# Kernel optimization log

Hardware: AMD Instinct MI355X
Metric: run time of the kernel (lower is better)

Reference implementation:

```python
import jax, jax.numpy as jnp
import numpy as np

B, S, IN, N, OUT = 4, 4096, 1024, 1024, 1024  # state_size == num_heads, head_dim = 1, hippo D = 1


def setup_inputs() -> dict:
    key = jax.random.key(0)
    ks = jax.random.split(key, 6)
    x = jax.random.normal(ks[0], (B, S, IN), dtype=jnp.float32)
    # input_projection: Linear(input_size, state_size, bias=True)
    Wi = jax.random.normal(ks[1], (IN, N), dtype=jnp.float32) / np.sqrt(IN)
    bi = jax.random.normal(ks[2], (N,), dtype=jnp.float32) * 0.01
    # state_weight (N,1,1) -> per-head scalar recurrence weight; hippo_weight (N,1) -> per-head scalar
    w = jax.random.normal(ks[3], (N,), dtype=jnp.float32)
    u = jax.random.normal(ks[4], (N,), dtype=jnp.float32)
    # output_projection: Linear(state_size, output_size, bias=False)
    Wo = jax.random.normal(ks[5], (N, OUT), dtype=jnp.float32) / np.sqrt(N)
    input_state = jnp.zeros((B, N), dtype=jnp.float32)         # (B, N, H=1) squeezed
    hippo_state = jnp.zeros((B, N, 1, 1), dtype=jnp.float32)   # (B, N, H=1, D=1)
    return {"x": x, "Wi": Wi, "bi": bi, "w": w, "u": u, "Wo": Wo,
            "input_state": input_state, "hippo_state": hippo_state}


def reference(x, Wi, bi, w, u, Wo, input_state, hippo_state):
    # input projection then split into N heads of dim 1 -> [B, S, N]
    xp = jnp.einsum("bsi,in->bsn", x, Wi) + bi
    # hippo cross-term: (hippo_state @ hippo_weight) with H=D=1 -> scalar per (b, n).
    # hippo_state is never updated inside the recurrence (torch path), so this is constant over time.
    hippo_term = hippo_state[..., 0, 0] * u  # [B, N]

    def step(h, xt):
        # h_t = tanh(h_{t-1} * w + x_t + hippo_term)   (per-head scalar recurrence, H=1)
        h = jnp.tanh(h * w + xt + hippo_term)
        return h, h

    xs = jnp.swapaxes(xp, 0, 1)  # [S, B, N]
    last_state, ys = jax.lax.scan(step, input_state, xs)
    states = jnp.swapaxes(ys, 0, 1)  # [B, S, N]
    out = jnp.einsum("bsn,no->bso", states, Wo)  # output_projection (no bias)
    output_state = last_state.reshape(B, -1)     # input[:, -1] flattened over (N, H)
    return out, output_state
```

## Files before the change

### kernel.cpp

```cpp
#include <hip/hip_runtime.h>
#include <hip/hip_bf16.h>

using f16x8 = __attribute__((ext_vector_type(8))) _Float16;
using f32x4 = __attribute__((ext_vector_type(4))) float;

extern "C" __device__ float __ocml_native_exp2_f32(float);

static constexpr int Bc = 4, Sc = 4096, INc = 1024, Nc = 1024, OUTc = 1024;
static constexpr int Mc = Bc * Sc;
#define K2LE 2.8853900817779268f

__device__ __forceinline__ unsigned short f2h(float f) {
    return __builtin_bit_cast(unsigned short, (_Float16)f);
}
__device__ __forceinline__ float h2f(unsigned short s) {
    return (float)__builtin_bit_cast(_Float16, s);
}

__global__ __launch_bounds__(256) void split2h(const float* __restrict__ in,
                                               unsigned short* __restrict__ hi,
                                               unsigned short* __restrict__ lo, int n4) {
    int i = blockIdx.x * blockDim.x + threadIdx.x;
    if (i >= n4) return;
    float4 v = reinterpret_cast<const float4*>(in)[i];
    ushort4 h, l;
    h.x = f2h(v.x); l.x = f2h(v.x - h2f(h.x));
    h.y = f2h(v.y); l.y = f2h(v.y - h2f(h.y));
    h.z = f2h(v.z); l.z = f2h(v.z - h2f(h.z));
    h.w = f2h(v.w); l.w = f2h(v.w - h2f(h.w));
    reinterpret_cast<ushort4*>(hi)[i] = h;
    reinterpret_cast<ushort4*>(lo)[i] = l;
}

__global__ __launch_bounds__(256) void tr_h2(const float* __restrict__ Wi,
                                             const float* __restrict__ Wo,
                                             unsigned short* __restrict__ WiT,
                                             unsigned short* __restrict__ WoT) {
    __shared__ float t[32][33];
    const float* in = blockIdx.z ? Wo : Wi;
    unsigned short* out = blockIdx.z ? WoT : WiT;
    int c0 = blockIdx.x * 32, r0 = blockIdx.y * 32;
    for (int i = threadIdx.y; i < 32; i += 8)
        t[i][threadIdx.x] = in[(size_t)(r0 + i) * 1024 + c0 + threadIdx.x];
    __syncthreads();
    for (int i = threadIdx.y; i < 32; i += 8)
        out[(size_t)(c0 + i) * 1024 + r0 + threadIdx.x] = f2h(t[threadIdx.x][i]);
}

template<int MODE>
__global__ __launch_bounds__(256) void gemm_h(const unsigned short* __restrict__ Ah,
                                              const unsigned short* __restrict__ Al,
                                              const unsigned short* __restrict__ BT,
                                              float* __restrict__ C, int N, int K,
                                              const float* __restrict__ bi,
                                              const float* __restrict__ u,
                                              const float* __restrict__ hs,
                                              const float* __restrict__ wv) {
    constexpr int BM = 128, BN = 128, BK = 64;
    __shared__ alignas(16) unsigned short Ash[BM * BK];
    __shared__ alignas(16) unsigned short Asl[MODE ? BM * BK : 1];
    __shared__ alignas(16) unsigned short Bs[BN * BK];
    const int nb = N >> 7;
    const int cpx = (int)gridDim.x >> 3;
    const int wg = (blockIdx.x & 7) * cpx + (blockIdx.x >> 3);
    const int bm = wg / nb, bn = wg % nb;
    const int tid = threadIdx.x;
    const int w = tid >> 6, l = tid & 63;
    const int wr = w >> 1, wc = w & 1;
    const int r = l & 15, g4 = l >> 4;
    const int lrow = l >> 3, lcol = (l & 7) * 8;

    f32x4 acc[4][4] = {};

    const size_t aoff = (size_t)bm * BM * K;
    const size_t boff = (size_t)bn * BN * K;

    for (int k0 = 0; k0 < K; k0 += BK) {
        __syncthreads();
#pragma unroll
        for (int i = 0; i < 4; i++) {
            size_t grow = (size_t)((w * 4 + i) * 8 + lrow) * K + (k0 + lcol);
            int ldst = (w * 4 + i) * 512;
            __builtin_amdgcn_global_load_lds(
                (const __attribute__((address_space(1))) void*)(Ah + aoff + grow),
                (__attribute__((address_space(3))) void*)(Ash + ldst), 16, 0, 0);
            if (MODE)
                __builtin_amdgcn_global_load_lds(
                    (const __attribute__((address_space(1))) void*)(Al + aoff + grow),
                    (__attribute__((address_space(3))) void*)(Asl + ldst), 16, 0, 0);
            __builtin_amdgcn_global_load_lds(
                (const __attribute__((address_space(1))) void*)(BT + boff + grow),
                (__attribute__((address_space(3))) void*)(Bs + ldst), 16, 0, 0);
        }
        __syncthreads();
#pragma unroll
        for (int kk = 0; kk < BK; kk += 32) {
            f16x8 ah[4], al[4], bf[4];
#pragma unroll
            for (int m = 0; m < 4; m++) {
                int off = (wr * 64 + m * 16 + r) * BK + kk + g4 * 8;
                ah[m] = *reinterpret_cast<const f16x8*>(Ash + off);
                if (MODE) al[m] = *reinterpret_cast<const f16x8*>(Asl + off);
            }
#pragma unroll
            for (int n = 0; n < 4; n++)
                bf[n] = *reinterpret_cast<const f16x8*>(Bs + (wc * 64 + n * 16 + r) * BK + kk + g4 * 8);
#pragma unroll
            for (int m = 0; m < 4; m++)
#pragma unroll
                for (int n = 0; n < 4; n++) {
                    acc[m][n] = __builtin_amdgcn_mfma_f32_16x16x32_f16(ah[m], bf[n], acc[m][n], 0, 0, 0);
                    if (MODE)
                        acc[m][n] = __builtin_amdgcn_mfma_f32_16x16x32_f16(al[m], bf[n], acc[m][n], 0, 0, 0);
                }
        }
    }

    const int bbase = MODE ? ((bm * BM) / Sc) * Nc : 0;
#pragma unroll
    for (int m = 0; m < 4; m++) {
        int row = bm * BM + wr * 64 + m * 16 + g4 * 4;
#pragma unroll
        for (int n = 0; n < 4; n++) {
            int col = bn * BN + wc * 64 + n * 16 + r;
            float extra = 0.f;
            if (MODE) extra = bi[col] + hs[bbase + col] * u[col] + wv[col];
#pragma unroll
            for (int q = 0; q < 4; q++) {
                float v = acc[m][n][q];
                if (MODE) v = (v + extra) * K2LE;
                C[(size_t)(row + q) * N + col] = v;
            }
        }
    }
}

static constexpr int SROW = 68;

template<bool PREF>
__device__ __forceinline__ void sblk(const float* __restrict__ xrow,
                                     float (&cur)[32], float (&nxt)[32],
                                     float* __restrict__ hbl, int tblk, float nw2, float& rr) {
#pragma unroll
    for (int d = 0; d < 32; d++) {
        if (PREF) nxt[d] = xrow[(size_t)(tblk + 32 + d) << 10];
        float z = fmaf(nw2, rr, cur[d]);
        float e = __ocml_native_exp2_f32(z);
        rr = __builtin_amdgcn_rcpf(e + 1.f);
        hbl[d * SROW] = rr;
    }
    asm volatile("s_waitcnt lgkmcnt(0)" ::: "memory");
    __builtin_amdgcn_s_barrier();
}

__device__ __forceinline__ unsigned int pk2(float a, float b) {
    return ((unsigned int)f2h(fmaf(-2.f, b, 1.f)) << 16) | f2h(fmaf(-2.f, a, 1.f));
}

__device__ __forceinline__ void drain(const float* __restrict__ buf, int tblk,
                                      unsigned short* __restrict__ srow, int n0, int l) {
    __builtin_amdgcn_s_barrier();
    asm volatile("" ::: "memory");
    int row8 = l >> 3, cg = l & 7;
#pragma unroll
    for (int i = 0; i < 4; i++) {
        int row = i * 8 + row8;
        float4 a = *reinterpret_cast<const float4*>(&buf[row * SROW + cg * 8]);
        float4 b = *reinterpret_cast<const float4*>(&buf[row * SROW + cg * 8 + 4]);
        uint4 v = { pk2(a.x, a.y), pk2(a.z, a.w), pk2(b.x, b.y), pk2(b.z, b.w) };
        *reinterpret_cast<uint4*>(&srow[((size_t)(tblk + row) << 10) + n0 + cg * 8]) = v;
    }
}

__global__ __launch_bounds__(128) void scan4(const float* __restrict__ xp,
                                             const float* __restrict__ w,
                                             const float* __restrict__ h0,
                                             unsigned short* __restrict__ states,
                                             float* __restrict__ out_state) {
    __shared__ alignas(16) float hb[2][32 * SROW];
    const int l = threadIdx.x & 63;
    const int wave = threadIdx.x >> 6;
    const int b = blockIdx.x >> 4;
    const int n0 = (blockIdx.x & 15) * 64;

    if (wave == 0) {
        const int tid = blockIdx.x * 64 + l;
        const int n = tid & (Nc - 1);
        float nw2 = w[n] * (-2.f * K2LE);
        float rr = 0.5f - 0.5f * h0[tid];
        const float* xrow = xp + ((size_t)b << 22) + n;
        float* hbl0 = &hb[0][l];
        float* hbl1 = &hb[1][l];

        float xa[32], xb[32];
#pragma unroll
        for (int d = 0; d < 32; d++) xa[d] = xrow[(size_t)d << 10];

        int t = 0;
        for (; t + 64 < Sc; t += 64) {
            sblk<true>(xrow, xa, xb, hbl0, t, nw2, rr);
            sblk<true>(xrow, xb, xa, hbl1, t + 32, nw2, rr);
        }
        sblk<true >(xrow, xa, xb, hbl0, t, nw2, rr);
        sblk<false>(xrow, xb, xa, hbl1, t + 32, nw2, rr);
        out_state[tid] = fmaf(-2.f, rr, 1.f);
    } else {
        unsigned short* srow = states + ((size_t)b << 22);
        for (int t = 0; t < Sc; t += 64) {
            drain(hb[0], t, srow, n0, l);
            drain(hb[1], t + 32, srow, n0, l);
        }
    }
}

extern "C" void kernel_launch(void* const* d_in, const int* in_sizes, int n_in,
                              void* d_out, int out_size, void* d_ws, size_t ws_size,
                              hipStream_t stream) {
    const float* x  = (const float*)d_in[0];
    const float* Wi = (const float*)d_in[1];
    const float* bi = (const float*)d_in[2];
    const float* w  = (const float*)d_in[3];
    const float* u  = (const float*)d_in[4];
    const float* Wo = (const float*)d_in[5];
    const float* h0 = (const float*)d_in[6];
    const float* hs = (const float*)d_in[7];
    float* out = (float*)d_out;
    float* out_state = out + (size_t)Mc * OUTc;
    float* xp = out;

    char* ws = (char*)d_ws;
    unsigned short* xh  = (unsigned short*)ws;
    unsigned short* xl  = (unsigned short*)(ws + 33554432);
    unsigned short* WiT = (unsigned short*)(ws + 67108864);
    unsigned short* WoT = (unsigned short*)(ws + 69206016);
    unsigned short* states = xh;

    split2h<<<(Mc * INc / 4 + 255) / 256, 256, 0, stream>>>(x, xh, xl, Mc * INc / 4);
    tr_h2<<<dim3(32, 32, 2), dim3(32, 8), 0, stream>>>(Wi, Wo, WiT, WoT);

    gemm_h<1><<<(Mc / 128) * (Nc / 128), 256, 0, stream>>>(xh, xl, WiT, xp, Nc, INc, bi, u, hs, w);
    scan4<<<64, 128, 0, stream>>>(xp, w, h0, states, out_state);
    gemm_h<0><<<(Mc / 128) * (OUTc / 128), 256, 0, stream>>>(states, nullptr, WoT, out, OUTc, Nc,
                                                             nullptr, nullptr, nullptr, nullptr);
}
```

Baseline: 254.3 us.

## Fuse fp32-to-fp16 hi/lo split of x into input projection GEMM

Removes the separate split2h pass that wrote fp16 hi and lo copies of x. The first GEMM now loads fp32 x directly through registers, splits each value into hi and lo halves, and stores both to LDS. This avoids a full read and write of the 64MB activation tensor and one launch. In exchange the A-tile load becomes a synchronous register path with no async global-to-LDS transfer, and every N-tile block redoes the conversion with twice the global bytes per A element.

```diff
diff --git a/kernel.cpp b/kernel.cpp
--- a/kernel.cpp
+++ b/kernel.cpp
@@ -15,21 +15,6 @@
 }
 __device__ __forceinline__ float h2f(unsigned short s) {
     return (float)__builtin_bit_cast(_Float16, s);
-}
-
-__global__ __launch_bounds__(256) void split2h(const float* __restrict__ in,
-                                               unsigned short* __restrict__ hi,
-                                               unsigned short* __restrict__ lo, int n4) {
-    int i = blockIdx.x * blockDim.x + threadIdx.x;
-    if (i >= n4) return;
-    float4 v = reinterpret_cast<const float4*>(in)[i];
-    ushort4 h, l;
-    h.x = f2h(v.x); l.x = f2h(v.x - h2f(h.x));
-    h.y = f2h(v.y); l.y = f2h(v.y - h2f(h.y));
-    h.z = f2h(v.z); l.z = f2h(v.z - h2f(h.z));
-    h.w = f2h(v.w); l.w = f2h(v.w - h2f(h.w));
-    reinterpret_cast<ushort4*>(hi)[i] = h;
-    reinterpret_cast<ushort4*>(lo)[i] = l;
 }
 
 __global__ __launch_bounds__(256) void tr_h2(const float* __restrict__ Wi,
@@ -48,8 +33,8 @@
 }
 
 template<int MODE>
-__global__ __launch_bounds__(256) void gemm_h(const unsigned short* __restrict__ Ah,
-                                              const unsigned short* __restrict__ Al,
+__global__ __launch_bounds__(256) void gemm_h(const unsigned short* __restrict__ Ah16,
+                                              const float* __restrict__ Af32,
                                               const unsigned short* __restrict__ BT,
                                               float* __restrict__ C, int N, int K,
                                               const float* __restrict__ bi,
@@ -72,7 +57,6 @@
 
     f32x4 acc[4][4] = {};
 
-    const size_t aoff = (size_t)bm * BM * K;
     const size_t boff = (size_t)bn * BN * K;
 
     for (int k0 = 0; k0 < K; k0 += BK) {
@@ -82,15 +66,38 @@
             size_t grow = (size_t)((w * 4 + i) * 8 + lrow) * K + (k0 + lcol);
             int ldst = (w * 4 + i) * 512;
             __builtin_amdgcn_global_load_lds(
-                (const __attribute__((address_space(1))) void*)(Ah + aoff + grow),
-                (__attribute__((address_space(3))) void*)(Ash + ldst), 16, 0, 0);
-            if (MODE)
-                __builtin_amdgcn_global_load_lds(
-                    (const __attribute__((address_space(1))) void*)(Al + aoff + grow),
-                    (__attribute__((address_space(3))) void*)(Asl + ldst), 16, 0, 0);
-            __builtin_amdgcn_global_load_lds(
                 (const __attribute__((address_space(1))) void*)(BT + boff + grow),
                 (__attribute__((address_space(3))) void*)(Bs + ldst), 16, 0, 0);
+        }
+        if (MODE) {
+            float4 av[8];
+#pragma unroll
+            for (int i = 0; i < 8; i++) {
+                int rg = (w * 8 + i) * 4 + (l >> 4);
+                av[i] = *reinterpret_cast<const float4*>(
+                    Af32 + (size_t)(bm * BM + rg) * K + k0 + (l & 15) * 4);
+            }
+#pragma unroll
+            for (int i = 0; i < 8; i++) {
+                int rg = (w * 8 + i) * 4 + (l >> 4);
+                int off = rg * BK + (l & 15) * 4;
+                float fx0 = av[i].x, fx1 = av[i].y, fx2 = av[i].z, fx3 = av[i].w;
+                unsigned short h0s = f2h(fx0), h1s = f2h(fx1), h2s = f2h(fx2), h3s = f2h(fx3);
+                ushort4 hh = { h0s, h1s, h2s, h3s };
+                ushort4 ll = { f2h(fx0 - h2f(h0s)), f2h(fx1 - h2f(h1s)),
+                               f2h(fx2 - h2f(h2s)), f2h(fx3 - h2f(h3s)) };
+                *reinterpret_cast<ushort4*>(Ash + off) = hh;
+                *reinterpret_cast<ushort4*>(Asl + off) = ll;
+            }
+        } else {
+            const size_t aoff = (size_t)bm * BM * K;
+#pragma unroll
+            for (int i = 0; i < 4; i++) {
+                size_t grow = (size_t)((w * 4 + i) * 8 + lrow) * K + (k0 + lcol);
+                __builtin_amdgcn_global_load_lds(
+                    (const __attribute__((address_space(1))) void*)(Ah16 + aoff + grow),
+                    (__attribute__((address_space(3))) void*)(Ash + (w * 4 + i) * 512), 16, 0, 0);
+            }
         }
         __syncthreads();
 #pragma unroll
@@ -229,16 +236,13 @@
     float* xp = out;
 
     char* ws = (char*)d_ws;
-    unsigned short* xh  = (unsigned short*)ws;
-    unsigned short* xl  = (unsigned short*)(ws + 33554432);
-    unsigned short* WiT = (unsigned short*)(ws + 67108864);
-    unsigned short* WoT = (unsigned short*)(ws + 69206016);
-    unsigned short* states = xh;
-
-    split2h<<<(Mc * INc / 4 + 255) / 256, 256, 0, stream>>>(x, xh, xl, Mc * INc / 4);
+    unsigned short* states = (unsigned short*)ws;
+    unsigned short* WiT = (unsigned short*)(ws + 33554432);
+    unsigned short* WoT = (unsigned short*)(ws + 35651584);
+
     tr_h2<<<dim3(32, 32, 2), dim3(32, 8), 0, stream>>>(Wi, Wo, WiT, WoT);
 
-    gemm_h<1><<<(Mc / 128) * (Nc / 128), 256, 0, stream>>>(xh, xl, WiT, xp, Nc, INc, bi, u, hs, w);
+    gemm_h<1><<<(Mc / 128) * (Nc / 128), 256, 0, stream>>>(nullptr, x, WiT, xp, Nc, INc, bi, u, hs, w);
     scan4<<<64, 128, 0, stream>>>(xp, w, h0, states, out_state);
     gemm_h<0><<<(Mc / 128) * (OUTc / 128), 256, 0, stream>>>(states, nullptr, WoT, out, OUTc, Nc,
                                                              nullptr, nullptr, nullptr, nullptr);
```

Measured after the change: 246.4 us. -3.1%, faster.
